# Optimization experiments

Hardware: AMD Instinct MI355X
Metric: run time of the kernel (lower is better)

Reference implementation:

```python
import jax, jax.numpy as jnp
import numpy as np

V, E, H2, K = 30000, 256, 256, 13  # vocab, embed dim, per-direction hidden, num tags
B, T = 64, 512


def setup_inputs() -> dict:
    key = jax.random.key(0)
    ks = jax.random.split(key, 12)
    s = 0.1
    return {
        "x": jax.random.randint(ks[0], (B, T), 0, V, dtype=jnp.int32),
        "emb": jax.random.normal(ks[1], (V, E), dtype=jnp.float32) * s,
        "w_ih_f": jax.random.normal(ks[2], (4 * H2, E), dtype=jnp.float32) * s,
        "w_hh_f": jax.random.normal(ks[3], (4 * H2, H2), dtype=jnp.float32) * s,
        "b_ih_f": jnp.zeros((4 * H2,), jnp.float32),
        "b_hh_f": jnp.zeros((4 * H2,), jnp.float32),
        "w_ih_b": jax.random.normal(ks[4], (4 * H2, E), dtype=jnp.float32) * s,
        "w_hh_b": jax.random.normal(ks[5], (4 * H2, H2), dtype=jnp.float32) * s,
        "b_ih_b": jnp.zeros((4 * H2,), jnp.float32),
        "b_hh_b": jnp.zeros((4 * H2,), jnp.float32),
        "w_out": jax.random.normal(ks[6], (K, 2 * H2), dtype=jnp.float32) * s,
        "b_out": jnp.zeros((K,), jnp.float32),
        "start_trans": jax.random.normal(ks[7], (K,), dtype=jnp.float32) * s,
        "end_trans": jax.random.normal(ks[8], (K,), dtype=jnp.float32) * s,
        "trans": jax.random.normal(ks[9], (K, K), dtype=jnp.float32) * s,
    }


def _lstm_dir(xg, w_hh, reverse):
    # xg: [T, B, 4H] precomputed input-side gate pre-activations (PyTorch i|f|g|o order)
    Bsz, H = xg.shape[1], w_hh.shape[1]

    def step(carry, g_in):
        h, c = carry
        g = g_in + h @ w_hh.T
        i, f, gg, o = jnp.split(g, 4, axis=-1)
        c = jax.nn.sigmoid(f) * c + jax.nn.sigmoid(i) * jnp.tanh(gg)
        h = jax.nn.sigmoid(o) * jnp.tanh(c)
        return (h, c), h

    init = (jnp.zeros((Bsz, H), xg.dtype), jnp.zeros((Bsz, H), xg.dtype))
    _, hs = jax.lax.scan(step, init, xg, reverse=reverse)
    return hs  # [T, B, H]


def reference(x, emb, w_ih_f, w_hh_f, b_ih_f, b_hh_f, w_ih_b, w_hh_b, b_ih_b, b_hh_b,
              w_out, b_out, start_trans, end_trans, trans):
    e = emb[x].transpose(1, 0, 2)                     # [T, B, E] time-major
    xg_f = e @ w_ih_f.T + (b_ih_f + b_hh_f)           # [T, B, 4H] (fold both biases)
    xg_b = e @ w_ih_b.T + (b_ih_b + b_hh_b)
    h_f = _lstm_dir(xg_f, w_hh_f, reverse=False)
    h_b = _lstm_dir(xg_b, w_hh_b, reverse=True)
    h = jnp.concatenate([h_f, h_b], axis=-1)          # [T, B, 2H]; dropout = identity (eval)
    emissions = h @ w_out.T + b_out                   # [T, B, K]

    # CRF Viterbi decode (torchcrf semantics, full mask)
    score = start_trans + emissions[0]                # [B, K]

    def vstep(score, emit_t):
        s = score[:, :, None] + trans[None] + emit_t[:, None, :]  # [B, K_prev, K_next]
        return s.max(axis=1), s.argmax(axis=1)

    score, bps = jax.lax.scan(vstep, score, emissions[1:])        # bps: [T-1, B, K]
    score = score + end_trans
    best_last = jnp.argmax(score, axis=-1)            # [B]
    best_score = jnp.max(score, axis=-1)              # [B]

    def btstep(tag, bp_t):
        prev = jnp.take_along_axis(bp_t, tag[:, None], axis=1)[:, 0]
        return prev, prev

    _, path_head = jax.lax.scan(btstep, best_last, bps, reverse=True)  # [T-1, B]
    path = jnp.concatenate([path_head, best_last[None]], axis=0).T     # [B, T]
    return path, best_score
```

## Files before the change

### kernel.cpp

```cpp
#include <hip/hip_runtime.h>
#include <stdint.h>
#include <stddef.h>

#define T_LEN  512
#define BATCH  64
#define NTAG   13
#define CT     64
#define NCHUNK 8

__device__ __forceinline__ float sigm(float x) { return 1.0f / (1.0f + expf(-x)); }

__global__ __launch_bounds__(256) void xg_gemm(
    const int* __restrict__ x, const float* __restrict__ emb,
    const float* __restrict__ w_ih_f, const float* __restrict__ w_ih_b,
    const float* __restrict__ b_ih_f, const float* __restrict__ b_hh_f,
    const float* __restrict__ b_ih_b, const float* __restrict__ b_hh_b,
    float* __restrict__ xg_ws, int chunk)
{
    const int tid = threadIdx.x;
    const int mt = blockIdx.x;
    const int nt = blockIdx.y;
    const int d  = blockIdx.z;
    const int tbase = (d == 0 ? chunk : (NCHUNK - 1 - chunk)) * CT;
    const float* W  = (d == 0) ? w_ih_f : w_ih_b;
    const float* bi = (d == 0) ? b_ih_f : b_ih_b;
    const float* bh = (d == 0) ? b_hh_f : b_hh_b;

    __shared__ __align__(16) float Wl[16][132];
    __shared__ __align__(16) float El[16][132];
    __shared__ int tok[128];

    if (tid < 128) {
        int col = nt * 128 + tid;
        tok[tid] = x[(col & 63) * T_LEN + tbase + (col >> 6)];
    }
    __syncthreads();

    const int r  = tid >> 1;
    const int c8 = (tid & 1) * 8;
    const int tm = tid >> 4;
    const int tn = tid & 15;

    float acc[8][8];
#pragma unroll
    for (int i = 0; i < 8; i++)
#pragma unroll
        for (int jz = 0; jz < 8; jz++) acc[i][jz] = 0.0f;

    const float* wrow = &W[(size_t)(mt * 128 + r) * 256];
    const float* erow = &emb[(size_t)tok[r] * 256];

    for (int kb = 0; kb < 256; kb += 16) {
        float4 w0 = *(const float4*)&wrow[kb + c8];
        float4 w1 = *(const float4*)&wrow[kb + c8 + 4];
        float4 e0 = *(const float4*)&erow[kb + c8];
        float4 e1 = *(const float4*)&erow[kb + c8 + 4];
        __syncthreads();
        Wl[c8+0][r] = w0.x; Wl[c8+1][r] = w0.y; Wl[c8+2][r] = w0.z; Wl[c8+3][r] = w0.w;
        Wl[c8+4][r] = w1.x; Wl[c8+5][r] = w1.y; Wl[c8+6][r] = w1.z; Wl[c8+7][r] = w1.w;
        El[c8+0][r] = e0.x; El[c8+1][r] = e0.y; El[c8+2][r] = e0.z; El[c8+3][r] = e0.w;
        El[c8+4][r] = e1.x; El[c8+5][r] = e1.y; El[c8+6][r] = e1.z; El[c8+7][r] = e1.w;
        __syncthreads();
#pragma unroll
        for (int kk = 0; kk < 16; kk++) {
            float a[8], b[8];
            *(float4*)&a[0] = *(const float4*)&Wl[kk][tm*8];
            *(float4*)&a[4] = *(const float4*)&Wl[kk][tm*8+4];
            *(float4*)&b[0] = *(const float4*)&El[kk][tn*8];
            *(float4*)&b[4] = *(const float4*)&El[kk][tn*8+4];
#pragma unroll
            for (int i = 0; i < 8; i++)
#pragma unroll
                for (int jz = 0; jz < 8; jz++)
                    acc[i][jz] += a[i] * b[jz];
        }
    }

    const int colbase = nt * 128 + tn * 8;
    const int j  = colbase >> 6;
    const int b0 = colbase & 63;
#pragma unroll
    for (int gi = 0; gi < 8; gi++) {
        int g = mt * 128 + tm * 8 + gi;
        float bias = bi[g] + bh[g];
        float* dst = &xg_ws[(((size_t)(d * CT + j) * 1024 + g) << 6) + b0];
        float4 v0 = make_float4(acc[gi][0]+bias, acc[gi][1]+bias, acc[gi][2]+bias, acc[gi][3]+bias);
        float4 v1 = make_float4(acc[gi][4]+bias, acc[gi][5]+bias, acc[gi][6]+bias, acc[gi][7]+bias);
        *(float4*)dst       = v0;
        *(float4*)(dst + 4) = v1;
    }
}

__global__ __launch_bounds__(256) void lstm_chunk(
    const float* __restrict__ xg_ws,
    const float* __restrict__ w_hh_f, const float* __restrict__ w_hh_b,
    float* h_ex, float* c_state, float* h_all, int* flags, int chunk)
{
    const int tid = threadIdx.x;
    const int bid = blockIdx.x;
    const int dg    = bid & 7;
    const int slice = bid >> 3;
    const int dir = dg & 1;
    const int grp = dg >> 1;
    const int h_base = slice * 8;
    const int sbase  = grp * 16;

    __shared__ __align__(16) float w_lds[32][260];
    __shared__ __align__(16) float h_lds[16][260];
    __shared__ __align__(16) float red[7][32][20];
    __shared__ float gatebuf[32][17];

    const float* W = dir ? w_hh_b : w_hh_f;
    for (int idx = tid; idx < 2048; idx += 256) {
        int f  = idx << 2;
        int rr = f >> 8;
        int c4 = f & 255;
        int row = (rr >> 3) * 256 + h_base + (rr & 7);
        *(float4*)&w_lds[rr][c4] = *(const float4*)&W[(size_t)row * 256 + c4];
    }

    const int ih_g = tid & 7;
    const int s_g  = tid >> 3;
    float c_val = 0.0f;
    if (tid < 128)
        c_val = c_state[(size_t)(dir * 64 + sbase + s_g) * 256 + h_base + ih_g];

    {
        const float* base = &h_ex[((size_t)dg * 16) * 256];
#pragma unroll
        for (int i = 0; i < 8; i++) {
            int pos = tid + 256 * i;
            int fo  = pos << 1;
            unsigned long long u64 = __hip_atomic_load(
                (const unsigned long long*)(base + fo), __ATOMIC_RELAXED, __HIP_MEMORY_SCOPE_AGENT);
            float2 v = __builtin_bit_cast(float2, u64);
            *(float2*)&h_lds[fo >> 8][fo & 255] = v;
        }
    }
    __syncthreads();

    const int kc   = tid >> 5;
    const int tile = tid & 31;
    const int gt = tile >> 2;
    const int st = tile & 3;
    const float* wr[4] = { &w_lds[gt][0], &w_lds[8+gt][0], &w_lds[16+gt][0], &w_lds[24+gt][0] };
    const float* hr[4] = { &h_lds[st][0], &h_lds[4+st][0], &h_lds[8+st][0],  &h_lds[12+st][0] };

    float hv_prev = 0.0f;
    size_t ha_prev = 0;

#pragma unroll 1
    for (int tl = 0; tl < CT; tl++) {
        const int jslot = dir ? (CT - 1 - tl) : tl;
        const int t = (dir ? (NCHUNK - 1 - chunk) : chunk) * CT + jslot;
        const int sc = chunk * CT + tl + 1;
        const int par = sc & 1;

        float xg0 = 0.f, xg1 = 0.f, xg2 = 0.f, xg3 = 0.f;
        if (tid < 128) {
            if (tl > 0) h_all[ha_prev] = hv_prev;
            const float* xp = &xg_ws[(((size_t)(dir * CT + jslot) * 1024) + h_base + ih_g) * 64 + sbase + s_g];
            xg0 = xp[0];
            xg1 = xp[1 * 256 * 64];
            xg2 = xp[2 * 256 * 64];
            xg3 = xp[3 * 256 * 64];
        }

        float acc[4][4];
#pragma unroll
        for (int gi = 0; gi < 4; gi++)
#pragma unroll
            for (int si = 0; si < 4; si++) acc[gi][si] = 0.0f;

        const int j0 = kc * 32;
#pragma unroll
        for (int m = 0; m < 8; m++) {
            const int jj = j0 + m * 4;
            float4 w4[4], h4[4];
#pragma unroll
            for (int i = 0; i < 4; i++) w4[i] = *(const float4*)(wr[i] + jj);
#pragma unroll
            for (int i = 0; i < 4; i++) h4[i] = *(const float4*)(hr[i] + jj);
#pragma unroll
            for (int gi = 0; gi < 4; gi++)
#pragma unroll
                for (int si = 0; si < 4; si++)
                    acc[gi][si] += w4[gi].x*h4[si].x + w4[gi].y*h4[si].y
                                 + w4[gi].z*h4[si].z + w4[gi].w*h4[si].w;
        }

        if (kc >= 1) {
#pragma unroll
            for (int gi = 0; gi < 4; gi++)
                *(float4*)&red[kc-1][tile][gi*4] =
                    make_float4(acc[gi][0], acc[gi][1], acc[gi][2], acc[gi][3]);
        }
        __syncthreads();
        if (kc == 0) {
#pragma unroll
            for (int p = 0; p < 7; p++)
#pragma unroll
                for (int gi = 0; gi < 4; gi++) {
                    float4 v = *(const float4*)&red[p][tile][gi*4];
                    acc[gi][0] += v.x; acc[gi][1] += v.y; acc[gi][2] += v.z; acc[gi][3] += v.w;
                }
#pragma unroll
            for (int gi = 0; gi < 4; gi++)
#pragma unroll
                for (int si = 0; si < 4; si++)
                    gatebuf[8*gi + gt][4*si + st] = acc[gi][si];
        }
        __syncthreads();

        if (tid < 128) {
            float gI = gatebuf[     ih_g][s_g] + xg0;
            float gF = gatebuf[8  + ih_g][s_g] + xg1;
            float gG = gatebuf[16 + ih_g][s_g] + xg2;
            float gO = gatebuf[24 + ih_g][s_g] + xg3;
            c_val = sigm(gF) * c_val + sigm(gI) * tanhf(gG);
            float hv = sigm(gO) * tanhf(c_val);
            __hip_atomic_store(&h_ex[(((size_t)par * 8 + dg) * 16 + s_g) * 256 + h_base + ih_g],
                               hv, __ATOMIC_RELAXED, __HIP_MEMORY_SCOPE_AGENT);
            hv_prev = hv;
            ha_prev = ((size_t)t * 64 + sbase + s_g) * 512 + dir * 256 + h_base + ih_g;
        }
        __syncthreads();

        if (tid == 0)
            __hip_atomic_store(&flags[dg * 32 + slice], sc, __ATOMIC_RELAXED, __HIP_MEMORY_SCOPE_AGENT);

        if (tid < 64) {
            const int* fp = &flags[dg * 32 + (tid & 31)];
            int spins = 0;
            int v = __hip_atomic_load(fp, __ATOMIC_RELAXED, __HIP_MEMORY_SCOPE_AGENT);
            while (__ballot(v < sc) != 0ull) {
                if (++spins > 8) __builtin_amdgcn_s_sleep(1);
                v = __hip_atomic_load(fp, __ATOMIC_RELAXED, __HIP_MEMORY_SCOPE_AGENT);
                if (spins > (1 << 20)) break;
            }
        }
        __syncthreads();

        {
            const float* base = &h_ex[(((size_t)par * 8 + dg) * 16) * 256];
#pragma unroll
            for (int i = 0; i < 8; i++) {
                int pos = tid + 256 * i;
                int fo  = pos << 1;
                unsigned long long u64 = __hip_atomic_load(
                    (const unsigned long long*)(base + fo), __ATOMIC_RELAXED, __HIP_MEMORY_SCOPE_AGENT);
                float2 v = __builtin_bit_cast(float2, u64);
                *(float2*)&h_lds[fo >> 8][fo & 255] = v;
            }
        }
        __syncthreads();
    }

    if (tid < 128) {
        h_all[ha_prev] = hv_prev;
        c_state[(size_t)(dir * 64 + sbase + s_g) * 256 + h_base + ih_g] = c_val;
    }
}

__global__ __launch_bounds__(256) void emis_kernel(
    const float* __restrict__ h_all, const float* __restrict__ w_out,
    const float* __restrict__ b_out, float* __restrict__ emis)
{
    const int row = blockIdx.x * 16 + (threadIdx.x >> 4);
    const int k   = threadIdx.x & 15;
    const float* hr = &h_all[(size_t)row * 512];
    const float* wr = &w_out[(size_t)(k < NTAG ? k : 0) * 512];
    float acc = 0.0f;
#pragma unroll 8
    for (int e = 0; e < 512; e += 4) {
        float4 h4 = *(const float4*)&hr[e];
        float4 w4 = *(const float4*)&wr[e];
        acc += h4.x*w4.x + h4.y*w4.y + h4.z*w4.z + h4.w*w4.w;
    }
    if (k < NTAG) emis[(size_t)row * NTAG + k] = acc + b_out[k];
}

__global__ __launch_bounds__(64) void viterbi_kernel(
    const float* __restrict__ emis, const float* __restrict__ start_trans,
    const float* __restrict__ end_trans, const float* __restrict__ trans,
    float* __restrict__ out)
{
    const int b = blockIdx.x;
    const int k = threadIdx.x;
    __shared__ float em[T_LEN * NTAG];
    __shared__ unsigned char bp[T_LEN][16];

    for (int t = k; t < T_LEN; t += 64) {
        const float* src = &emis[((size_t)t * 64 + b) * NTAG];
#pragma unroll
        for (int kk = 0; kk < NTAG; kk++)
            em[t * NTAG + kk] = src[kk];
    }
    __syncthreads();

    float tc[NTAG];
#pragma unroll
    for (int kp = 0; kp < NTAG; kp++)
        tc[kp] = (k < NTAG) ? trans[kp * NTAG + k] : 0.0f;

    float score = (k < NTAG) ? (start_trans[k] + em[k]) : -3.0e38f;

    for (int t = 1; t < T_LEN; t++) {
        float best = -3.0e38f;
        int bi = 0;
#pragma unroll
        for (int kp = 0; kp < NTAG; kp++) {
            float v = __shfl(score, kp) + tc[kp];
            if (v > best) { best = v; bi = kp; }
        }
        if (k < NTAG) {
            score = best + em[t * NTAG + k];
            bp[t][k] = (unsigned char)bi;
        }
    }
    if (k < NTAG) score += end_trans[k];
    else score = -3.0e38f;
    __syncthreads();

    float bs = -3.0e38f;
    int tag = 0;
#pragma unroll
    for (int kk = 0; kk < NTAG; kk++) {
        float v = __shfl(score, kk);
        if (v > bs) { bs = v; tag = kk; }
    }
    if (k == 0) {
        out[32768 + b] = bs;
        int tg = tag;
        out[b * T_LEN + (T_LEN - 1)] = (float)tg;
        for (int t = T_LEN - 1; t >= 1; t--) {
            tg = bp[t][tg];
            out[b * T_LEN + t - 1] = (float)tg;
        }
    }
}

extern "C" void kernel_launch(void* const* d_in, const int* in_sizes, int n_in,
                              void* d_out, int out_size, void* d_ws, size_t ws_size,
                              hipStream_t stream)
{
    (void)in_sizes; (void)n_in; (void)out_size; (void)ws_size;
    const int*   x    = (const int*)  d_in[0];
    const float* emb  = (const float*)d_in[1];
    const float* wihf = (const float*)d_in[2];
    const float* whhf = (const float*)d_in[3];
    const float* bihf = (const float*)d_in[4];
    const float* bhhf = (const float*)d_in[5];
    const float* wihb = (const float*)d_in[6];
    const float* whhb = (const float*)d_in[7];
    const float* bihb = (const float*)d_in[8];
    const float* bhhb = (const float*)d_in[9];
    const float* wout = (const float*)d_in[10];
    const float* bout = (const float*)d_in[11];
    const float* stt  = (const float*)d_in[12];
    const float* ent  = (const float*)d_in[13];
    const float* trn  = (const float*)d_in[14];
    float* out = (float*)d_out;

    char* ws = (char*)d_ws;
    size_t off = 0;
    float* xg_ws = (float*)(ws + off); off += (size_t)2 * CT * 1024 * 64 * 4;
    float* h_all = (float*)(ws + off); off += (size_t)T_LEN * 64 * 512 * 4;
    float* h_ex  = (float*)(ws + off); off += (size_t)2 * 8 * 16 * 256 * 4;
    float* c_st  = (float*)(ws + off); off += (size_t)2 * 64 * 256 * 4;
    float* emis  = (float*)(ws + off); off += (size_t)T_LEN * 64 * NTAG * 4;
    int*   flags = (int*)  (ws + off); off += 8 * 32 * 4;

    hipMemsetAsync(h_ex,  0, (size_t)2 * 8 * 16 * 256 * 4, stream);
    hipMemsetAsync(c_st,  0, (size_t)2 * 64 * 256 * 4, stream);
    hipMemsetAsync(flags, 0, 8 * 32 * 4, stream);

    for (int c = 0; c < NCHUNK; c++) {
        xg_gemm<<<dim3(8, 32, 2), 256, 0, stream>>>(x, emb, wihf, wihb,
                                                    bihf, bhhf, bihb, bhhb, xg_ws, c);
        lstm_chunk<<<256, 256, 0, stream>>>(xg_ws, whhf, whhb, h_ex, c_st, h_all, flags, c);
    }
    emis_kernel<<<2048, 256, 0, stream>>>(h_all, wout, bout, emis);
    viterbi_kernel<<<64, 64, 0, stream>>>(emis, stt, ent, trn, out);
}
```

Measured before the change: 3.458 ms.

## Precompute all input gates in one GEMM and run a single persistent LSTM kernel

```diff
diff --git a/kernel.cpp b/kernel.cpp
--- a/kernel.cpp
+++ b/kernel.cpp
@@ -9,6 +9,249 @@
 #define NCHUNK 8
 
 __device__ __forceinline__ float sigm(float x) { return 1.0f / (1.0f + expf(-x)); }
+
+__global__ __launch_bounds__(256) void xg_gemm_all(
+    const int* __restrict__ x, const float* __restrict__ emb,
+    const float* __restrict__ w_ih_f, const float* __restrict__ w_ih_b,
+    const float* __restrict__ b_ih_f, const float* __restrict__ b_hh_f,
+    const float* __restrict__ b_ih_b, const float* __restrict__ b_hh_b,
+    float* __restrict__ xg_ws)
+{
+    const int tid = threadIdx.x;
+    const int mt = blockIdx.x;
+    const int nt = blockIdx.y;
+    const int chunk = blockIdx.z & 7;
+    const int d     = blockIdx.z >> 3;
+    const int tbase = (d == 0 ? chunk : (NCHUNK - 1 - chunk)) * CT;
+    const float* W  = (d == 0) ? w_ih_f : w_ih_b;
+    const float* bi = (d == 0) ? b_ih_f : b_ih_b;
+    const float* bh = (d == 0) ? b_hh_f : b_hh_b;
+
+    __shared__ __align__(16) float Wl[16][132];
+    __shared__ __align__(16) float El[16][132];
+    __shared__ int tok[128];
+
+    if (tid < 128) {
+        int col = nt * 128 + tid;
+        tok[tid] = x[(col & 63) * T_LEN + tbase + (col >> 6)];
+    }
+    __syncthreads();
+
+    const int r  = tid >> 1;
+    const int c8 = (tid & 1) * 8;
+    const int tm = tid >> 4;
+    const int tn = tid & 15;
+
+    float acc[8][8];
+#pragma unroll
+    for (int i = 0; i < 8; i++)
+#pragma unroll
+        for (int jz = 0; jz < 8; jz++) acc[i][jz] = 0.0f;
+
+    const float* wrow = &W[(size_t)(mt * 128 + r) * 256];
+    const float* erow = &emb[(size_t)tok[r] * 256];
+
+    for (int kb = 0; kb < 256; kb += 16) {
+        float4 w0 = *(const float4*)&wrow[kb + c8];
+        float4 w1 = *(const float4*)&wrow[kb + c8 + 4];
+        float4 e0 = *(const float4*)&erow[kb + c8];
+        float4 e1 = *(const float4*)&erow[kb + c8 + 4];
+        __syncthreads();
+        Wl[c8+0][r] = w0.x; Wl[c8+1][r] = w0.y; Wl[c8+2][r] = w0.z; Wl[c8+3][r] = w0.w;
+        Wl[c8+4][r] = w1.x; Wl[c8+5][r] = w1.y; Wl[c8+6][r] = w1.z; Wl[c8+7][r] = w1.w;
+        El[c8+0][r] = e0.x; El[c8+1][r] = e0.y; El[c8+2][r] = e0.z; El[c8+3][r] = e0.w;
+        El[c8+4][r] = e1.x; El[c8+5][r] = e1.y; El[c8+6][r] = e1.z; El[c8+7][r] = e1.w;
+        __syncthreads();
+#pragma unroll
+        for (int kk = 0; kk < 16; kk++) {
+            float a[8], b[8];
+            *(float4*)&a[0] = *(const float4*)&Wl[kk][tm*8];
+            *(float4*)&a[4] = *(const float4*)&Wl[kk][tm*8+4];
+            *(float4*)&b[0] = *(const float4*)&El[kk][tn*8];
+            *(float4*)&b[4] = *(const float4*)&El[kk][tn*8+4];
+#pragma unroll
+            for (int i = 0; i < 8; i++)
+#pragma unroll
+                for (int jz = 0; jz < 8; jz++)
+                    acc[i][jz] += a[i] * b[jz];
+        }
+    }
+
+    const int colbase = nt * 128 + tn * 8;
+    const int j  = colbase >> 6;
+    const int b0 = colbase & 63;
+    const int tg = tbase + j;
+#pragma unroll
+    for (int gi = 0; gi < 8; gi++) {
+        int g = mt * 128 + tm * 8 + gi;
+        float bias = bi[g] + bh[g];
+        float* dst = &xg_ws[(((size_t)(d * T_LEN + tg) * 1024 + g) << 6) + b0];
+        float4 v0 = make_float4(acc[gi][0]+bias, acc[gi][1]+bias, acc[gi][2]+bias, acc[gi][3]+bias);
+        float4 v1 = make_float4(acc[gi][4]+bias, acc[gi][5]+bias, acc[gi][6]+bias, acc[gi][7]+bias);
+        *(float4*)dst       = v0;
+        *(float4*)(dst + 4) = v1;
+    }
+}
+
+__global__ __launch_bounds__(256) void lstm_full(
+    const float* __restrict__ xg_ws,
+    const float* __restrict__ w_hh_f, const float* __restrict__ w_hh_b,
+    float* h_ex, float* h_all, int* flags)
+{
+    const int tid = threadIdx.x;
+    const int bid = blockIdx.x;
+    const int dg    = bid & 7;
+    const int slice = bid >> 3;
+    const int dir = dg & 1;
+    const int grp = dg >> 1;
+    const int h_base = slice * 8;
+    const int sbase  = grp * 16;
+
+    __shared__ __align__(16) float w_lds[32][260];
+    __shared__ __align__(16) float h_lds[16][260];
+    __shared__ __align__(16) float red[7][32][20];
+    __shared__ float gatebuf[32][17];
+
+    const float* W = dir ? w_hh_b : w_hh_f;
+    for (int idx = tid; idx < 2048; idx += 256) {
+        int f  = idx << 2;
+        int rr = f >> 8;
+        int c4 = f & 255;
+        int row = (rr >> 3) * 256 + h_base + (rr & 7);
+        *(float4*)&w_lds[rr][c4] = *(const float4*)&W[(size_t)row * 256 + c4];
+    }
+
+    const int ih_g = tid & 7;
+    const int s_g  = tid >> 3;
+    float c_val = 0.0f;
+
+    {
+        for (int i = tid; i < 16 * 256; i += 256)
+            h_lds[i >> 8][i & 255] = 0.0f;
+    }
+    __syncthreads();
+
+    const int kc   = tid >> 5;
+    const int tile = tid & 31;
+    const int gt = tile >> 2;
+    const int st = tile & 3;
+    const float* wr[4] = { &w_lds[gt][0], &w_lds[8+gt][0], &w_lds[16+gt][0], &w_lds[24+gt][0] };
+    const float* hr[4] = { &h_lds[st][0], &h_lds[4+st][0], &h_lds[8+st][0],  &h_lds[12+st][0] };
+
+    float hv_prev = 0.0f;
+    size_t ha_prev = 0;
+
+#pragma unroll 1
+    for (int tl = 0; tl < T_LEN; tl++) {
+        const int t  = dir ? (T_LEN - 1 - tl) : tl;
+        const int sc = tl + 1;
+        const int par = sc & 1;
+
+        float xg0 = 0.f, xg1 = 0.f, xg2 = 0.f, xg3 = 0.f;
+        if (tid < 128) {
+            if (tl > 0) h_all[ha_prev] = hv_prev;
+            const float* xp = &xg_ws[(((size_t)(dir * T_LEN + t) * 1024) + h_base + ih_g) * 64 + sbase + s_g];
+            xg0 = xp[0];
+            xg1 = xp[1 * 256 * 64];
+            xg2 = xp[2 * 256 * 64];
+            xg3 = xp[3 * 256 * 64];
+        }
+
+        float acc[4][4];
+#pragma unroll
+        for (int gi = 0; gi < 4; gi++)
+#pragma unroll
+            for (int si = 0; si < 4; si++) acc[gi][si] = 0.0f;
+
+        const int j0 = kc * 32;
+#pragma unroll
+        for (int m = 0; m < 8; m++) {
+            const int jj = j0 + m * 4;
+            float4 w4[4], h4[4];
+#pragma unroll
+            for (int i = 0; i < 4; i++) w4[i] = *(const float4*)(wr[i] + jj);
+#pragma unroll
+            for (int i = 0; i < 4; i++) h4[i] = *(const float4*)(hr[i] + jj);
+#pragma unroll
+            for (int gi = 0; gi < 4; gi++)
+#pragma unroll
+                for (int si = 0; si < 4; si++)
+                    acc[gi][si] += w4[gi].x*h4[si].x + w4[gi].y*h4[si].y
+                                 + w4[gi].z*h4[si].z + w4[gi].w*h4[si].w;
+        }
+
+        if (kc >= 1) {
+#pragma unroll
+            for (int gi = 0; gi < 4; gi++)
+                *(float4*)&red[kc-1][tile][gi*4] =
+                    make_float4(acc[gi][0], acc[gi][1], acc[gi][2], acc[gi][3]);
+        }
+        __syncthreads();
+        if (kc == 0) {
+#pragma unroll
+            for (int p = 0; p < 7; p++)
+#pragma unroll
+                for (int gi = 0; gi < 4; gi++) {
+                    float4 v = *(const float4*)&red[p][tile][gi*4];
+                    acc[gi][0] += v.x; acc[gi][1] += v.y; acc[gi][2] += v.z; acc[gi][3] += v.w;
+                }
+#pragma unroll
+            for (int gi = 0; gi < 4; gi++)
+#pragma unroll
+                for (int si = 0; si < 4; si++)
+                    gatebuf[8*gi + gt][4*si + st] = acc[gi][si];
+        }
+        __syncthreads();
+
+        if (tid < 128) {
+            float gI = gatebuf[     ih_g][s_g] + xg0;
+            float gF = gatebuf[8  + ih_g][s_g] + xg1;
+            float gG = gatebuf[16 + ih_g][s_g] + xg2;
+            float gO = gatebuf[24 + ih_g][s_g] + xg3;
+            c_val = sigm(gF) * c_val + sigm(gI) * tanhf(gG);
+            float hv = sigm(gO) * tanhf(c_val);
+            __hip_atomic_store(&h_ex[(((size_t)par * 8 + dg) * 16 + s_g) * 256 + h_base + ih_g],
+                               hv, __ATOMIC_RELAXED, __HIP_MEMORY_SCOPE_AGENT);
+            hv_prev = hv;
+            ha_prev = ((size_t)t * 64 + sbase + s_g) * 512 + dir * 256 + h_base + ih_g;
+        }
+        __syncthreads();
+
+        if (tl != T_LEN - 1) {
+            if (tid == 0)
+                __hip_atomic_store(&flags[dg * 32 + slice], sc, __ATOMIC_RELAXED, __HIP_MEMORY_SCOPE_AGENT);
+
+            if (tid < 64) {
+                const int* fp = &flags[dg * 32 + (tid & 31)];
+                int spins = 0;
+                int v = __hip_atomic_load(fp, __ATOMIC_RELAXED, __HIP_MEMORY_SCOPE_AGENT);
+                while (__ballot(v < sc) != 0ull) {
+                    if (++spins > 8) __builtin_amdgcn_s_sleep(1);
+                    v = __hip_atomic_load(fp, __ATOMIC_RELAXED, __HIP_MEMORY_SCOPE_AGENT);
+                    if (spins > (1 << 20)) break;
+                }
+            }
+            __syncthreads();
+
+            {
+                const float* base = &h_ex[(((size_t)par * 8 + dg) * 16) * 256];
+#pragma unroll
+                for (int i = 0; i < 8; i++) {
+                    int pos = tid + 256 * i;
+                    int fo  = pos << 1;
+                    unsigned long long u64 = __hip_atomic_load(
+                        (const unsigned long long*)(base + fo), __ATOMIC_RELAXED, __HIP_MEMORY_SCOPE_AGENT);
+                    float2 v = __builtin_bit_cast(float2, u64);
+                    *(float2*)&h_lds[fo >> 8][fo & 255] = v;
+                }
+            }
+            __syncthreads();
+        }
+    }
+
+    if (tid < 128)
+        h_all[ha_prev] = hv_prev;
+}
 
 __global__ __launch_bounds__(256) void xg_gemm(
     const int* __restrict__ x, const float* __restrict__ emb,
@@ -344,7 +587,7 @@
                               void* d_out, int out_size, void* d_ws, size_t ws_size,
                               hipStream_t stream)
 {
-    (void)in_sizes; (void)n_in; (void)out_size; (void)ws_size;
+    (void)in_sizes; (void)n_in; (void)out_size;
     const int*   x    = (const int*)  d_in[0];
     const float* emb  = (const float*)d_in[1];
     const float* wihf = (const float*)d_in[2];
@@ -362,23 +605,41 @@
     const float* trn  = (const float*)d_in[14];
     float* out = (float*)d_out;
 
+    const size_t XG_FULL_BYTES = (size_t)2 * T_LEN * 1024 * 64 * 4;
+    const size_t XG_CHUNK_BYTES= (size_t)2 * CT * 1024 * 64 * 4;
+    const size_t HALL_BYTES    = (size_t)T_LEN * 64 * 512 * 4;
+    const size_t HEX_BYTES     = (size_t)2 * 8 * 16 * 256 * 4;
+    const size_t CST_BYTES     = (size_t)2 * 64 * 256 * 4;
+    const size_t EMIS_BYTES    = (size_t)T_LEN * 64 * NTAG * 4;
+    const size_t FLAG_BYTES    = 8 * 32 * 4;
+
+    const size_t need_full = XG_FULL_BYTES + HALL_BYTES + HEX_BYTES
+                           + CST_BYTES + EMIS_BYTES + FLAG_BYTES;
+    const bool full = (ws_size == 0) || (ws_size >= need_full);
+
     char* ws = (char*)d_ws;
     size_t off = 0;
-    float* xg_ws = (float*)(ws + off); off += (size_t)2 * CT * 1024 * 64 * 4;
-    float* h_all = (float*)(ws + off); off += (size_t)T_LEN * 64 * 512 * 4;
-    float* h_ex  = (float*)(ws + off); off += (size_t)2 * 8 * 16 * 256 * 4;
-    float* c_st  = (float*)(ws + off); off += (size_t)2 * 64 * 256 * 4;
-    float* emis  = (float*)(ws + off); off += (size_t)T_LEN * 64 * NTAG * 4;
-    int*   flags = (int*)  (ws + off); off += 8 * 32 * 4;
-
-    hipMemsetAsync(h_ex,  0, (size_t)2 * 8 * 16 * 256 * 4, stream);
-    hipMemsetAsync(c_st,  0, (size_t)2 * 64 * 256 * 4, stream);
-    hipMemsetAsync(flags, 0, 8 * 32 * 4, stream);
-
-    for (int c = 0; c < NCHUNK; c++) {
-        xg_gemm<<<dim3(8, 32, 2), 256, 0, stream>>>(x, emb, wihf, wihb,
-                                                    bihf, bhhf, bihb, bhhb, xg_ws, c);
-        lstm_chunk<<<256, 256, 0, stream>>>(xg_ws, whhf, whhb, h_ex, c_st, h_all, flags, c);
+    float* xg_ws = (float*)(ws + off); off += full ? XG_FULL_BYTES : XG_CHUNK_BYTES;
+    float* h_all = (float*)(ws + off); off += HALL_BYTES;
+    float* h_ex  = (float*)(ws + off); off += HEX_BYTES;
+    float* c_st  = (float*)(ws + off); off += CST_BYTES;
+    float* emis  = (float*)(ws + off); off += EMIS_BYTES;
+    int*   flags = (int*)  (ws + off); off += FLAG_BYTES;
+
+    hipMemsetAsync(flags, 0, FLAG_BYTES, stream);
+
+    if (full) {
+        xg_gemm_all<<<dim3(8, 32, 16), 256, 0, stream>>>(x, emb, wihf, wihb,
+                                                         bihf, bhhf, bihb, bhhb, xg_ws);
+        lstm_full<<<256, 256, 0, stream>>>(xg_ws, whhf, whhb, h_ex, h_all, flags);
+    } else {
+        hipMemsetAsync(h_ex, 0, HEX_BYTES, stream);
+        hipMemsetAsync(c_st, 0, CST_BYTES, stream);
+        for (int c = 0; c < NCHUNK; c++) {
+            xg_gemm<<<dim3(8, 32, 2), 256, 0, stream>>>(x, emb, wihf, wihb,
+                                                        bihf, bhhf, bihb, bhhb, xg_ws, c);
+            lstm_chunk<<<256, 256, 0, stream>>>(xg_ws, whhf, whhb, h_ex, c_st, h_all, flags, c);
+        }
     }
     emis_kernel<<<2048, 256, 0, stream>>>(h_all, wout, bout, emis);
     viterbi_kernel<<<64, 64, 0, stream>>>(emis, stt, ent, trn, out);
```

Result: no change. 3.457 ms (-0.0%).

## Fuse input-gate projection into persistent LSTM kernel, overlapping with flag spin-wait

Applied to the files above, without the earlier changes.

```diff
diff --git a/kernel.cpp b/kernel.cpp
--- a/kernel.cpp
+++ b/kernel.cpp
@@ -5,96 +5,44 @@
 #define T_LEN  512
 #define BATCH  64
 #define NTAG   13
-#define CT     64
-#define NCHUNK 8
+#define CTS    128
+#define NSC    4
 
 __device__ __forceinline__ float sigm(float x) { return 1.0f / (1.0f + expf(-x)); }
 
-__global__ __launch_bounds__(256) void xg_gemm(
+__device__ __forceinline__ void xg_compute(
+    const float* __restrict__ wih,
+    const float* __restrict__ er,
+    float* __restrict__ xgout,
+    int r4, int s)
+{
+    const float* w0 = wih + (size_t)(     r4) * 260;
+    const float* w1 = wih + (size_t)( 8 + r4) * 260;
+    const float* w2 = wih + (size_t)(16 + r4) * 260;
+    const float* w3 = wih + (size_t)(24 + r4) * 260;
+    float a0 = 0.f, a1 = 0.f, a2 = 0.f, a3 = 0.f;
+#pragma unroll 8
+    for (int k = 0; k < 256; k += 4) {
+        float4 e4 = *(const float4*)&er[k];
+        float4 q;
+        q = *(const float4*)&w0[k]; a0 += q.x*e4.x; a0 += q.y*e4.y; a0 += q.z*e4.z; a0 += q.w*e4.w;
+        q = *(const float4*)&w1[k]; a1 += q.x*e4.x; a1 += q.y*e4.y; a1 += q.z*e4.z; a1 += q.w*e4.w;
+        q = *(const float4*)&w2[k]; a2 += q.x*e4.x; a2 += q.y*e4.y; a2 += q.z*e4.z; a2 += q.w*e4.w;
+        q = *(const float4*)&w3[k]; a3 += q.x*e4.x; a3 += q.y*e4.y; a3 += q.z*e4.z; a3 += q.w*e4.w;
+    }
+    xgout[(size_t)(     r4) * 17 + s] = a0;
+    xgout[(size_t)( 8 + r4) * 17 + s] = a1;
+    xgout[(size_t)(16 + r4) * 17 + s] = a2;
+    xgout[(size_t)(24 + r4) * 17 + s] = a3;
+}
+
+__global__ __launch_bounds__(256) void lstm_fused(
     const int* __restrict__ x, const float* __restrict__ emb,
+    const float* __restrict__ w_hh_f, const float* __restrict__ w_hh_b,
     const float* __restrict__ w_ih_f, const float* __restrict__ w_ih_b,
     const float* __restrict__ b_ih_f, const float* __restrict__ b_hh_f,
     const float* __restrict__ b_ih_b, const float* __restrict__ b_hh_b,
-    float* __restrict__ xg_ws, int chunk)
-{
-    const int tid = threadIdx.x;
-    const int mt = blockIdx.x;
-    const int nt = blockIdx.y;
-    const int d  = blockIdx.z;
-    const int tbase = (d == 0 ? chunk : (NCHUNK - 1 - chunk)) * CT;
-    const float* W  = (d == 0) ? w_ih_f : w_ih_b;
-    const float* bi = (d == 0) ? b_ih_f : b_ih_b;
-    const float* bh = (d == 0) ? b_hh_f : b_hh_b;
-
-    __shared__ __align__(16) float Wl[16][132];
-    __shared__ __align__(16) float El[16][132];
-    __shared__ int tok[128];
-
-    if (tid < 128) {
-        int col = nt * 128 + tid;
-        tok[tid] = x[(col & 63) * T_LEN + tbase + (col >> 6)];
-    }
-    __syncthreads();
-
-    const int r  = tid >> 1;
-    const int c8 = (tid & 1) * 8;
-    const int tm = tid >> 4;
-    const int tn = tid & 15;
-
-    float acc[8][8];
-#pragma unroll
-    for (int i = 0; i < 8; i++)
-#pragma unroll
-        for (int jz = 0; jz < 8; jz++) acc[i][jz] = 0.0f;
-
-    const float* wrow = &W[(size_t)(mt * 128 + r) * 256];
-    const float* erow = &emb[(size_t)tok[r] * 256];
-
-    for (int kb = 0; kb < 256; kb += 16) {
-        float4 w0 = *(const float4*)&wrow[kb + c8];
-        float4 w1 = *(const float4*)&wrow[kb + c8 + 4];
-        float4 e0 = *(const float4*)&erow[kb + c8];
-        float4 e1 = *(const float4*)&erow[kb + c8 + 4];
-        __syncthreads();
-        Wl[c8+0][r] = w0.x; Wl[c8+1][r] = w0.y; Wl[c8+2][r] = w0.z; Wl[c8+3][r] = w0.w;
-        Wl[c8+4][r] = w1.x; Wl[c8+5][r] = w1.y; Wl[c8+6][r] = w1.z; Wl[c8+7][r] = w1.w;
-        El[c8+0][r] = e0.x; El[c8+1][r] = e0.y; El[c8+2][r] = e0.z; El[c8+3][r] = e0.w;
-        El[c8+4][r] = e1.x; El[c8+5][r] = e1.y; El[c8+6][r] = e1.z; El[c8+7][r] = e1.w;
-        __syncthreads();
-#pragma unroll
-        for (int kk = 0; kk < 16; kk++) {
-            float a[8], b[8];
-            *(float4*)&a[0] = *(const float4*)&Wl[kk][tm*8];
-            *(float4*)&a[4] = *(const float4*)&Wl[kk][tm*8+4];
-            *(float4*)&b[0] = *(const float4*)&El[kk][tn*8];
-            *(float4*)&b[4] = *(const float4*)&El[kk][tn*8+4];
-#pragma unroll
-            for (int i = 0; i < 8; i++)
-#pragma unroll
-                for (int jz = 0; jz < 8; jz++)
-                    acc[i][jz] += a[i] * b[jz];
-        }
-    }
-
-    const int colbase = nt * 128 + tn * 8;
-    const int j  = colbase >> 6;
-    const int b0 = colbase & 63;
-#pragma unroll
-    for (int gi = 0; gi < 8; gi++) {
-        int g = mt * 128 + tm * 8 + gi;
-        float bias = bi[g] + bh[g];
-        float* dst = &xg_ws[(((size_t)(d * CT + j) * 1024 + g) << 6) + b0];
-        float4 v0 = make_float4(acc[gi][0]+bias, acc[gi][1]+bias, acc[gi][2]+bias, acc[gi][3]+bias);
-        float4 v1 = make_float4(acc[gi][4]+bias, acc[gi][5]+bias, acc[gi][6]+bias, acc[gi][7]+bias);
-        *(float4*)dst       = v0;
-        *(float4*)(dst + 4) = v1;
-    }
-}
-
-__global__ __launch_bounds__(256) void lstm_chunk(
-    const float* __restrict__ xg_ws,
-    const float* __restrict__ w_hh_f, const float* __restrict__ w_hh_b,
-    float* h_ex, float* c_state, float* h_all, int* flags, int chunk)
+    float* h_ex, float* c_state, float* h_all, int* flags, int sch)
 {
     const int tid = threadIdx.x;
     const int bid = blockIdx.x;
@@ -106,24 +54,50 @@
     const int sbase  = grp * 16;
 
     __shared__ __align__(16) float w_lds[32][260];
+    __shared__ __align__(16) float wih_lds[32][260];
     __shared__ __align__(16) float h_lds[16][260];
+    __shared__ __align__(16) float e_lds[2][16][260];
     __shared__ __align__(16) float red[7][32][20];
     __shared__ float gatebuf[32][17];
-
-    const float* W = dir ? w_hh_b : w_hh_f;
+    __shared__ float xg_lds[2][32][17];
+
+    const float* Whh = dir ? w_hh_b : w_hh_f;
+    const float* Wih = dir ? w_ih_b : w_ih_f;
+    const float* bi  = dir ? b_ih_b : b_ih_f;
+    const float* bh  = dir ? b_hh_b : b_hh_f;
+
+    const int tA = (dir ? (NSC - 1 - sch) : sch) * CTS;
+
     for (int idx = tid; idx < 2048; idx += 256) {
         int f  = idx << 2;
         int rr = f >> 8;
         int c4 = f & 255;
         int row = (rr >> 3) * 256 + h_base + (rr & 7);
-        *(float4*)&w_lds[rr][c4] = *(const float4*)&W[(size_t)row * 256 + c4];
+        *(float4*)&w_lds[rr][c4]   = *(const float4*)&Whh[(size_t)row * 256 + c4];
+        *(float4*)&wih_lds[rr][c4] = *(const float4*)&Wih[(size_t)row * 256 + c4];
     }
 
     const int ih_g = tid & 7;
     const int s_g  = tid >> 3;
     float c_val = 0.0f;
-    if (tid < 128)
+    float bias_g[4] = {0.f, 0.f, 0.f, 0.f};
+    if (tid < 128) {
         c_val = c_state[(size_t)(dir * 64 + sbase + s_g) * 256 + h_base + ih_g];
+#pragma unroll
+        for (int q = 0; q < 4; q++) {
+            int g = q * 256 + h_base + ih_g;
+            bias_g[q] = bi[g] + bh[g];
+        }
+#pragma unroll
+        for (int L = 0; L < 2; L++) {
+            int tg  = tA + (dir ? (CTS - 1 - L) : L);
+            int tok = x[(sbase + s_g) * T_LEN + tg];
+            const float4* src = (const float4*)&emb[(size_t)tok * 256 + ih_g * 32];
+            float4* dst = (float4*)&e_lds[L][s_g][ih_g * 32];
+#pragma unroll
+            for (int j = 0; j < 8; j++) dst[j] = src[j];
+        }
+    }
 
     {
         const float* base = &h_ex[((size_t)dg * 16) * 256];
@@ -139,6 +113,12 @@
     }
     __syncthreads();
 
+    if (tid >= 128) {
+        int u = tid - 128;
+        xg_compute(&wih_lds[0][0], &e_lds[0][u & 15][0], &xg_lds[0][0][0], u >> 4, u & 15);
+    }
+    __syncthreads();
+
     const int kc   = tid >> 5;
     const int tile = tid & 31;
     const int gt = tile >> 2;
@@ -150,20 +130,23 @@
     size_t ha_prev = 0;
 
 #pragma unroll 1
-    for (int tl = 0; tl < CT; tl++) {
-        const int jslot = dir ? (CT - 1 - tl) : tl;
-        const int t = (dir ? (NCHUNK - 1 - chunk) : chunk) * CT + jslot;
-        const int sc = chunk * CT + tl + 1;
+    for (int tl = 0; tl < CTS; tl++) {
+        const int t  = tA + (dir ? (CTS - 1 - tl) : tl);
+        const int sc = sch * CTS + tl + 1;
         const int par = sc & 1;
-
-        float xg0 = 0.f, xg1 = 0.f, xg2 = 0.f, xg3 = 0.f;
+        const int cb  = tl & 1;
+        const bool epref = (tl + 2 < CTS);
+
+        float4 ereg[8];
         if (tid < 128) {
             if (tl > 0) h_all[ha_prev] = hv_prev;
-            const float* xp = &xg_ws[(((size_t)(dir * CT + jslot) * 1024) + h_base + ih_g) * 64 + sbase + s_g];
-            xg0 = xp[0];
-            xg1 = xp[1 * 256 * 64];
-            xg2 = xp[2 * 256 * 64];
-            xg3 = xp[3 * 256 * 64];
+            if (epref) {
+                int t2  = tA + (dir ? (CTS - 1 - (tl + 2)) : (tl + 2));
+                int tok = x[(sbase + s_g) * T_LEN + t2];
+                const float4* src = (const float4*)&emb[(size_t)tok * 256 + ih_g * 32];
+#pragma unroll
+                for (int j = 0; j < 8; j++) ereg[j] = src[j];
+            }
         }
 
         float acc[4][4];
@@ -213,10 +196,14 @@
         __syncthreads();
 
         if (tid < 128) {
-            float gI = gatebuf[     ih_g][s_g] + xg0;
-            float gF = gatebuf[8  + ih_g][s_g] + xg1;
-            float gG = gatebuf[16 + ih_g][s_g] + xg2;
-            float gO = gatebuf[24 + ih_g][s_g] + xg3;
+            float xgi = xg_lds[cb][     ih_g][s_g] + bias_g[0];
+            float xgf = xg_lds[cb][ 8 + ih_g][s_g] + bias_g[1];
+            float xgg = xg_lds[cb][16 + ih_g][s_g] + bias_g[2];
+            float xgo = xg_lds[cb][24 + ih_g][s_g] + bias_g[3];
+            float gI = gatebuf[     ih_g][s_g] + xgi;
+            float gF = gatebuf[ 8 + ih_g][s_g] + xgf;
+            float gG = gatebuf[16 + ih_g][s_g] + xgg;
+            float gO = gatebuf[24 + ih_g][s_g] + xgo;
             c_val = sigm(gF) * c_val + sigm(gI) * tanhf(gG);
             float hv = sigm(gO) * tanhf(c_val);
             __hip_atomic_store(&h_ex[(((size_t)par * 8 + dg) * 16 + s_g) * 256 + h_base + ih_g],
@@ -229,7 +216,13 @@
         if (tid == 0)
             __hip_atomic_store(&flags[dg * 32 + slice], sc, __ATOMIC_RELAXED, __HIP_MEMORY_SCOPE_AGENT);
 
-        if (tid < 64) {
+        if (tid >= 128) {
+            if (tl + 1 < CTS) {
+                int u = tid - 128;
+                xg_compute(&wih_lds[0][0], &e_lds[(tl + 1) & 1][u & 15][0],
+                           &xg_lds[(tl + 1) & 1][0][0], u >> 4, u & 15);
+            }
+        } else if (tid < 64) {
             const int* fp = &flags[dg * 32 + (tid & 31)];
             int spins = 0;
             int v = __hip_atomic_load(fp, __ATOMIC_RELAXED, __HIP_MEMORY_SCOPE_AGENT);
@@ -241,16 +234,21 @@
         }
         __syncthreads();
 
-        {
+        if (tid < 128) {
             const float* base = &h_ex[(((size_t)par * 8 + dg) * 16) * 256];
 #pragma unroll
-            for (int i = 0; i < 8; i++) {
-                int pos = tid + 256 * i;
+            for (int i = 0; i < 16; i++) {
+                int pos = tid + 128 * i;
                 int fo  = pos << 1;
                 unsigned long long u64 = __hip_atomic_load(
                     (const unsigned long long*)(base + fo), __ATOMIC_RELAXED, __HIP_MEMORY_SCOPE_AGENT);
                 float2 v = __builtin_bit_cast(float2, u64);
                 *(float2*)&h_lds[fo >> 8][fo & 255] = v;
+            }
+            if (epref) {
+                float4* dst = (float4*)&e_lds[tl & 1][s_g][ih_g * 32];
+#pragma unroll
+                for (int j = 0; j < 8; j++) dst[j] = ereg[j];
             }
         }
         __syncthreads();
@@ -362,24 +360,29 @@
     const float* trn  = (const float*)d_in[14];
     float* out = (float*)d_out;
 
+    const size_t HALL_BYTES = (size_t)T_LEN * 64 * 512 * 4;
+    const size_t HEX_BYTES  = (size_t)2 * 8 * 16 * 256 * 4;
+    const size_t CST_BYTES  = (size_t)2 * 64 * 256 * 4;
+    const size_t EMIS_BYTES = (size_t)T_LEN * 64 * NTAG * 4;
+    const size_t FLAG_BYTES = 8 * 32 * 4;
+
     char* ws = (char*)d_ws;
     size_t off = 0;
-    float* xg_ws = (float*)(ws + off); off += (size_t)2 * CT * 1024 * 64 * 4;
-    float* h_all = (float*)(ws + off); off += (size_t)T_LEN * 64 * 512 * 4;
-    float* h_ex  = (float*)(ws + off); off += (size_t)2 * 8 * 16 * 256 * 4;
-    float* c_st  = (float*)(ws + off); off += (size_t)2 * 64 * 256 * 4;
-    float* emis  = (float*)(ws + off); off += (size_t)T_LEN * 64 * NTAG * 4;
-    int*   flags = (int*)  (ws + off); off += 8 * 32 * 4;
-
-    hipMemsetAsync(h_ex,  0, (size_t)2 * 8 * 16 * 256 * 4, stream);
-    hipMemsetAsync(c_st,  0, (size_t)2 * 64 * 256 * 4, stream);
-    hipMemsetAsync(flags, 0, 8 * 32 * 4, stream);
-
-    for (int c = 0; c < NCHUNK; c++) {
-        xg_gemm<<<dim3(8, 32, 2), 256, 0, stream>>>(x, emb, wihf, wihb,
-                                                    bihf, bhhf, bihb, bhhb, xg_ws, c);
-        lstm_chunk<<<256, 256, 0, stream>>>(xg_ws, whhf, whhb, h_ex, c_st, h_all, flags, c);
-    }
+    float* h_all = (float*)(ws + off); off += HALL_BYTES;
+    float* h_ex  = (float*)(ws + off); off += HEX_BYTES;
+    float* c_st  = (float*)(ws + off); off += CST_BYTES;
+    float* emis  = (float*)(ws + off); off += EMIS_BYTES;
+    int*   flags = (int*)  (ws + off); off += FLAG_BYTES;
+
+    hipMemsetAsync(h_ex,  0, HEX_BYTES, stream);
+    hipMemsetAsync(c_st,  0, CST_BYTES, stream);
+    hipMemsetAsync(flags, 0, FLAG_BYTES, stream);
+
+    for (int c = 0; c < NSC; c++)
+        lstm_fused<<<256, 256, 0, stream>>>(x, emb, whhf, whhb, wihf, wihb,
+                                            bihf, bhhf, bihb, bhhb,
+                                            h_ex, c_st, h_all, flags, c);
+
     emis_kernel<<<2048, 256, 0, stream>>>(h_all, wout, bout, emis);
     viterbi_kernel<<<64, 64, 0, stream>>>(emis, stt, ent, trn, out);
 }
```

After: 7.721 ms. 123% more time.
